# Kernel optimization log

Hardware: AMD Instinct MI355X
Metric: run time of the kernel (lower is better)

## Reference

```python
import jax, jax.numpy as jnp
import numpy as np
import math

N_EMBD = 1024
BLOCK_SIZE = 2048
B = 4

def setup_inputs() -> dict:
    key = jax.random.key(0)
    ks = jax.random.split(key, 9)
    s = 0.02
    return {
        "q": jax.random.normal(ks[0], (B, BLOCK_SIZE, N_EMBD), jnp.float32),
        "k": jax.random.normal(ks[1], (B, BLOCK_SIZE, N_EMBD), jnp.float32),
        "v": jax.random.normal(ks[2], (B, BLOCK_SIZE, N_EMBD), jnp.float32),
        "wq_w": jax.random.normal(ks[3], (N_EMBD, N_EMBD), jnp.float32) * s,
        "wq_b": jax.random.normal(ks[4], (N_EMBD,), jnp.float32) * s,
        "wk_w": jax.random.normal(ks[5], (N_EMBD, N_EMBD), jnp.float32) * s,
        "wk_b": jax.random.normal(ks[6], (N_EMBD,), jnp.float32) * s,
        "wv_w": jax.random.normal(ks[7], (N_EMBD, N_EMBD), jnp.float32) * s,
        "wv_b": jax.random.normal(ks[8], (N_EMBD,), jnp.float32) * s,
        "causal": 1,
    }

def reference(q, k, v, wq_w, wq_b, wk_w, wk_b, wv_w, wv_b, causal):
    # torch Linear: y = x @ W.T + b
    qp = jnp.einsum('bte,oe->bto', q, wq_w) + wq_b
    kp = jnp.einsum('bte,oe->bto', k, wk_w) + wk_b
    vp = jnp.einsum('bte,oe->bto', v, wv_w) + wv_b
    scale = 1.0 / math.sqrt(N_EMBD)
    weights = jnp.einsum('bqe,bke->bqk', qp, kp) * scale  # [B,T1,T2]
    if causal:
        T1, T2 = qp.shape[1], kp.shape[1]
        mask = jnp.tril(jnp.ones((T1, T2), dtype=bool))
        weights = jnp.where(mask, weights, -jnp.inf)
    attn = jax.nn.softmax(weights, axis=-1)
    return jnp.einsum('bqk,bke->bqe', attn, vp)
```

## Files before the change

### kernel.cpp

```cpp
#include <hip/hip_runtime.h>
#include <hip/hip_bf16.h>
#include <cstdint>
#include <math.h>

#define T 2048
#define NE 1024
#define NB 4

typedef __attribute__((ext_vector_type(8))) short short8;
typedef __attribute__((ext_vector_type(4))) float floatx4;

__device__ __forceinline__ unsigned short f2bf(float f) {
    unsigned u = __float_as_uint(f);
    u += 0x7FFF + ((u >> 16) & 1);
    return (unsigned short)(u >> 16);
}

__device__ __forceinline__ short8 cvt8(floatx4 f0, floatx4 f1) {
    __hip_bfloat162 a = __float22bfloat162_rn(float2{f0[0], f0[1]});
    __hip_bfloat162 b = __float22bfloat162_rn(float2{f0[2], f0[3]});
    __hip_bfloat162 c = __float22bfloat162_rn(float2{f1[0], f1[1]});
    __hip_bfloat162 d = __float22bfloat162_rn(float2{f1[2], f1[3]});
    union { short8 s; unsigned u[4]; } r;
    r.u[0] = *(unsigned*)&a; r.u[1] = *(unsigned*)&b;
    r.u[2] = *(unsigned*)&c; r.u[3] = *(unsigned*)&d;
    return r.s;
}

__device__ __forceinline__ void gl2lds(const void* g, void* l) {
    __builtin_amdgcn_global_load_lds(
        (const __attribute__((address_space(1))) void*)g,
        (__attribute__((address_space(3))) void*)l, 16, 0, 0);
}

template<int BIAS_MODE, bool OUT_F32, bool CKLIM, bool DUAL, int MODE>
__global__ __launch_bounds__(256) void gemm_bf16(
    const unsigned short* __restrict__ A0, const unsigned short* __restrict__ A1,
    const unsigned short* __restrict__ B0, const unsigned short* __restrict__ B1,
    const float* __restrict__ bias0, const float* __restrict__ bias1,
    void* __restrict__ C0, void* __restrict__ C1,
    int K, int lda, int ldb, int ldc,
    size_t sA, size_t sB, size_t sC, float scale)
{
    int tm, tn;
    const int bz = blockIdx.z;
    if (MODE == 2) {
        const int i = blockIdx.x;
        int lin = (i & 7) * 17 + (i >> 3);
        tm = (int)((sqrtf(8.f * (float)lin + 1.f) - 1.f) * 0.5f);
        while ((tm + 1) * (tm + 2) / 2 <= lin) ++tm;
        while (tm * (tm + 1) / 2 > lin) --tm;
        tn = lin - tm * (tm + 1) / 2;
    } else if (MODE == 1) {
        const int bid = blockIdx.x;
        const int lin = (bid & 7) * (gridDim.x >> 3) + (bid >> 3);
        tm = lin >> 3; tn = lin & 7;
    } else if (MODE == 3) {
        const int xcd = blockIdx.x & 7, j = blockIdx.x >> 3;
        tm = (j & 1) ? xcd : (15 - xcd);
        tn = j >> 1;
    } else {
        tn = blockIdx.x; tm = blockIdx.y;
    }

    __shared__ __align__(16) char As[16384];
    __shared__ __align__(16) char Bs[16384];

    const int tid = threadIdx.x, lane = tid & 63, wave = tid >> 6;
    const int wm = wave & 1, wn = wave >> 1;
    const int quad = lane >> 4, l15 = lane & 15;

    const char* Ab = (const char*)((DUAL && bz) ? A1 : A0) + (size_t)bz * sA * 2;
    const char* Bb = (const char*)((DUAL && bz) ? B1 : B0) + (size_t)bz * sB * 2;
    const float* bias = (DUAL && bz) ? bias1 : bias0;

    int Keff = K;
    if (CKLIM) { int kl = (tm + 1) * 128; Keff = kl < K ? kl : K; }

    const size_t ldab = (size_t)lda * 2, ldbb = (size_t)ldb * 2;
    const char* gA = Ab + (size_t)(tm * 128 + wave * 8 + (lane >> 3)) * ldab + (size_t)(lane & 7) * 16;
    const char* gB = Bb + (size_t)(tn * 128 + wave * 8 + (lane >> 3)) * ldbb + (size_t)(lane & 7) * 16;
    char* lA = As + wave * 1024;
    char* lB = Bs + wave * 1024;

    floatx4 acc[4][4] = {};

    for (int k0 = 0; k0 < Keff; k0 += 64) {
        const size_t kb = (size_t)k0 * 2;
        #pragma unroll
        for (int c = 0; c < 4; ++c)
            gl2lds(gA + (size_t)c * 32 * ldab + kb, lA + c * 4096);
        #pragma unroll
        for (int c = 0; c < 4; ++c)
            gl2lds(gB + (size_t)c * 32 * ldbb + kb, lB + c * 4096);
        __syncthreads();

        #pragma unroll
        for (int kk = 0; kk < 2; kk++) {
            short8 af[4], bfr[4];
            #pragma unroll
            for (int i = 0; i < 4; i++)
                af[i] = *(const short8*)(As + (wm * 64 + i * 16 + l15) * 128 + kk * 64 + quad * 16);
            #pragma unroll
            for (int j = 0; j < 4; j++)
                bfr[j] = *(const short8*)(Bs + (wn * 64 + j * 16 + l15) * 128 + kk * 64 + quad * 16);
            #pragma unroll
            for (int i = 0; i < 4; i++)
                #pragma unroll
                for (int j = 0; j < 4; j++)
                    acc[i][j] = __builtin_amdgcn_mfma_f32_16x16x32_bf16(af[i], bfr[j], acc[i][j], 0, 0, 0);
        }
        __syncthreads();
    }

    char* Cb = (char*)((DUAL && bz) ? C1 : C0) + (size_t)bz * sC * (OUT_F32 ? 4 : 2);
    #pragma unroll
    for (int i = 0; i < 4; i++) {
        #pragma unroll
        for (int j = 0; j < 4; j++) {
            const int n = tn * 128 + wn * 64 + j * 16 + l15;
            #pragma unroll
            for (int r = 0; r < 4; r++) {
                const int m = tm * 128 + wm * 64 + i * 16 + quad * 4 + r;
                float val = acc[i][j][r] * scale;
                if (BIAS_MODE == 1) val += bias[n];
                if (BIAS_MODE == 2) val += bias[m];
                if (OUT_F32) ((float*)Cb)[(size_t)m * ldc + n] = val;
                else         ((unsigned short*)Cb)[(size_t)m * ldc + n] = f2bf(val);
            }
        }
    }
}

__global__ __launch_bounds__(256) void cvt_all(
    const float* __restrict__ q, const float* __restrict__ k, const float* __restrict__ v,
    const float* __restrict__ wq, const float* __restrict__ wk, const float* __restrict__ wv,
    unsigned short* __restrict__ qb, unsigned short* __restrict__ kb, unsigned short* __restrict__ vb,
    unsigned short* __restrict__ wqb, unsigned short* __restrict__ wkb, unsigned short* __restrict__ wvb)
{
    const int IN8 = NB * T * NE / 8;
    const int W8  = NE * NE / 8;
    int i = blockIdx.x * 256 + threadIdx.x;
    const float* s; unsigned short* d; int j;
    if (i < 3 * IN8) {
        int sel = i / IN8; j = i - sel * IN8;
        s = sel == 0 ? q : sel == 1 ? k : v;
        d = sel == 0 ? qb : sel == 1 ? kb : vb;
    } else {
        int t2 = i - 3 * IN8; int sel = t2 / W8; j = t2 - sel * W8;
        s = sel == 0 ? wq : sel == 1 ? wk : wv;
        d = sel == 0 ? wqb : sel == 1 ? wkb : wvb;
    }
    const floatx4* p = (const floatx4*)s;
    ((short8*)d)[j] = cvt8(p[2 * j], p[2 * j + 1]);
}

__global__ __launch_bounds__(256) void softmax_causal(unsigned short* __restrict__ S)
{
    const int row = blockIdx.x;
    const int b = row >> 11, r = row & 2047;
    unsigned short* p = S + ((size_t)b * T + (size_t)r) * T;
    const int nv = r + 1;
    const int lim = ((r >> 7) + 1) * 128;
    const int tid = threadIdx.x, lane = tid & 63, wave = tid >> 6;
    const int c0 = tid * 8;
    const bool act = c0 < lim;

    short8 raw = {};
    if (act) raw = ((const short8*)p)[tid];
    float x[8];
    float mx = -3.0e38f;
    #pragma unroll
    for (int j = 0; j < 8; j++) {
        float vv = -3.0e38f;
        if (c0 + j < nv) vv = __uint_as_float((unsigned)(unsigned short)raw[j] << 16);
        x[j] = vv;
        mx = fmaxf(mx, vv);
    }
    #pragma unroll
    for (int off = 32; off > 0; off >>= 1)
        mx = fmaxf(mx, __shfl_xor(mx, off));
    __shared__ float smax[4], ssum[4];
    if (lane == 0) smax[wave] = mx;
    __syncthreads();
    mx = fmaxf(fmaxf(smax[0], smax[1]), fmaxf(smax[2], smax[3]));

    float s = 0.f;
    #pragma unroll
    for (int j = 0; j < 8; j++) {
        float e = 0.f;
        if (c0 + j < nv) e = __expf(x[j] - mx);
        x[j] = e;
        s += e;
    }
    #pragma unroll
    for (int off = 32; off > 0; off >>= 1)
        s += __shfl_xor(s, off);
    if (lane == 0) ssum[wave] = s;
    __syncthreads();
    const float inv = 1.f / (ssum[0] + ssum[1] + ssum[2] + ssum[3]);

    if (act) {
        short8 o;
        #pragma unroll
        for (int j = 0; j < 8; j++)
            o[j] = (short)f2bf(x[j] * inv);
        ((short8*)p)[tid] = o;
    }
}

extern "C" void kernel_launch(void* const* d_in, const int* in_sizes, int n_in,
                              void* d_out, int out_size, void* d_ws, size_t ws_size,
                              hipStream_t stream)
{
    const float* q    = (const float*)d_in[0];
    const float* k    = (const float*)d_in[1];
    const float* v    = (const float*)d_in[2];
    const float* wq_w = (const float*)d_in[3];
    const float* wq_b = (const float*)d_in[4];
    const float* wk_w = (const float*)d_in[5];
    const float* wk_b = (const float*)d_in[6];
    const float* wv_w = (const float*)d_in[7];
    const float* wv_b = (const float*)d_in[8];

    const size_t INEL = (size_t)NB * T * NE;

    unsigned short* qp = (unsigned short*)d_out;
    unsigned short* kp = qp + INEL;

    unsigned short* vpT = (unsigned short*)d_ws;
    unsigned short* S   = vpT + (size_t)NB * NE * T;
    unsigned short* qb  = S;
    unsigned short* kb  = qb + INEL;
    unsigned short* vb  = kb + INEL;
    unsigned short* wqb = vb + INEL;
    unsigned short* wkb = wqb + (size_t)NE * NE;
    unsigned short* wvb = wkb + (size_t)NE * NE;

    dim3 blk(256);

    const int NCVT = (3 * (int)(INEL / 8) + 3 * NE * NE / 8 + 255) / 256;
    cvt_all<<<dim3(NCVT), blk, 0, stream>>>(q, k, v, wq_w, wk_w, wv_w, qb, kb, vb, wqb, wkb, wvb);

    gemm_bf16<1, false, false, true, 1><<<dim3(512, 1, 2), blk, 0, stream>>>(
        qb, kb, wqb, wkb, wq_b, wk_b, qp, kp, NE, NE, NE, NE, 0, 0, 0, 1.0f);

    gemm_bf16<2, false, false, false, 0><<<dim3(T/128, NE/128, NB), blk, 0, stream>>>(
        wvb, nullptr, vb, nullptr, wv_b, nullptr, vpT, nullptr,
        NE, NE, NE, T, 0, (size_t)T * NE, (size_t)NE * T, 1.0f);

    gemm_bf16<0, false, false, false, 2><<<dim3(136, 1, NB), blk, 0, stream>>>(
        qp, nullptr, kp, nullptr, nullptr, nullptr, S, nullptr,
        NE, NE, NE, T, (size_t)T * NE, (size_t)T * NE, (size_t)T * T, 0.03125f);

    softmax_causal<<<dim3(NB * T), blk, 0, stream>>>(S);

    gemm_bf16<0, true, true, false, 3><<<dim3(128, 1, NB), blk, 0, stream>>>(
        S, nullptr, vpT, nullptr, nullptr, nullptr, d_out, nullptr,
        T, T, T, NE, (size_t)T * T, (size_t)NE * T, (size_t)T * NE, 1.0f);
}
```

Baseline: 343.7 us.

## Swizzle LDS tiles with XOR and use 256x128 tiles for projection GEMMs

LDS chunk positions are XOR-swizzled by row so the MFMA fragment reads avoid bank conflicts. The GEMM is parameterised by waves per row, and the Q/K and V projection GEMMs now use 512-thread blocks with 256-row A tiles. This raises B-tile reuse and cuts the block count. The risk is fewer blocks for the V projection and higher register or LDS pressure per block.

```diff
diff --git a/kernel.cpp b/kernel.cpp
--- a/kernel.cpp
+++ b/kernel.cpp
@@ -33,15 +33,16 @@
         (__attribute__((address_space(3))) void*)l, 16, 0, 0);
 }
 
-template<int BIAS_MODE, bool OUT_F32, bool CKLIM, bool DUAL, int MODE>
-__global__ __launch_bounds__(256) void gemm_bf16(
+template<int NWROW, int BIAS_MODE, bool OUT_F32, bool CKLIM, bool DUAL, int MODE>
+__global__ __launch_bounds__(NWROW * 128, 4) void gemm_bf16(
     const unsigned short* __restrict__ A0, const unsigned short* __restrict__ A1,
     const unsigned short* __restrict__ B0, const unsigned short* __restrict__ B1,
     const float* __restrict__ bias0, const float* __restrict__ bias1,
     void* __restrict__ C0, void* __restrict__ C1,
     int K, int lda, int ldb, int ldc,
-    size_t sA, size_t sB, size_t sC, float scale)
-{
+    size_t sA, size_t sB, size_t sC, float scale, int ntnShift)
+{
+    constexpr int NTHR = NWROW * 128;
     int tm, tn;
     const int bz = blockIdx.z;
     if (MODE == 2) {
@@ -54,7 +55,7 @@
     } else if (MODE == 1) {
         const int bid = blockIdx.x;
         const int lin = (bid & 7) * (gridDim.x >> 3) + (bid >> 3);
-        tm = lin >> 3; tn = lin & 7;
+        tm = lin >> ntnShift; tn = lin & ((1 << ntnShift) - 1);
     } else if (MODE == 3) {
         const int xcd = blockIdx.x & 7, j = blockIdx.x >> 3;
         tm = (j & 1) ? xcd : (15 - xcd);
@@ -63,12 +64,14 @@
         tn = blockIdx.x; tm = blockIdx.y;
     }
 
-    __shared__ __align__(16) char As[16384];
-    __shared__ __align__(16) char Bs[16384];
+    __shared__ __align__(16) char As[NWROW * 64 * 128];
+    __shared__ __align__(16) char Bs[128 * 128];
 
     const int tid = threadIdx.x, lane = tid & 63, wave = tid >> 6;
-    const int wm = wave & 1, wn = wave >> 1;
+    const int wm = wave % NWROW, wn = wave / NWROW;
     const int quad = lane >> 4, l15 = lane & 15;
+    const int p = l15 & 7;
+    const int r8 = lane >> 3, c8 = lane & 7;
 
     const char* Ab = (const char*)((DUAL && bz) ? A1 : A0) + (size_t)bz * sA * 2;
     const char* Bb = (const char*)((DUAL && bz) ? B1 : B0) + (size_t)bz * sB * 2;
@@ -78,10 +81,11 @@
     if (CKLIM) { int kl = (tm + 1) * 128; Keff = kl < K ? kl : K; }
 
     const size_t ldab = (size_t)lda * 2, ldbb = (size_t)ldb * 2;
-    const char* gA = Ab + (size_t)(tm * 128 + wave * 8 + (lane >> 3)) * ldab + (size_t)(lane & 7) * 16;
-    const char* gB = Bb + (size_t)(tn * 128 + wave * 8 + (lane >> 3)) * ldbb + (size_t)(lane & 7) * 16;
+    const char* gA = Ab + (size_t)(tm * (NWROW * 64) + wave * 8 + r8) * ldab + (size_t)((c8 ^ r8) * 16);
+    const char* gB = Bb + (size_t)(tn * 128 + wave * 8 + r8) * ldbb + (size_t)((c8 ^ r8) * 16);
     char* lA = As + wave * 1024;
     char* lB = Bs + wave * 1024;
+    constexpr int BCALLS = 8 / NWROW;
 
     floatx4 acc[4][4] = {};
 
@@ -89,10 +93,10 @@
         const size_t kb = (size_t)k0 * 2;
         #pragma unroll
         for (int c = 0; c < 4; ++c)
-            gl2lds(gA + (size_t)c * 32 * ldab + kb, lA + c * 4096);
-        #pragma unroll
-        for (int c = 0; c < 4; ++c)
-            gl2lds(gB + (size_t)c * 32 * ldbb + kb, lB + c * 4096);
+            gl2lds(gA + (size_t)(c * NWROW * 16) * ldab + kb, lA + c * NTHR * 16);
+        #pragma unroll
+        for (int c = 0; c < BCALLS; ++c)
+            gl2lds(gB + (size_t)(c * NWROW * 16) * ldbb + kb, lB + c * NTHR * 16);
         __syncthreads();
 
         #pragma unroll
@@ -100,10 +104,10 @@
             short8 af[4], bfr[4];
             #pragma unroll
             for (int i = 0; i < 4; i++)
-                af[i] = *(const short8*)(As + (wm * 64 + i * 16 + l15) * 128 + kk * 64 + quad * 16);
+                af[i] = *(const short8*)(As + (wm * 64 + i * 16 + l15) * 128 + (((kk * 4 + quad) ^ p) << 4));
             #pragma unroll
             for (int j = 0; j < 4; j++)
-                bfr[j] = *(const short8*)(Bs + (wn * 64 + j * 16 + l15) * 128 + kk * 64 + quad * 16);
+                bfr[j] = *(const short8*)(Bs + (wn * 64 + j * 16 + l15) * 128 + (((kk * 4 + quad) ^ p) << 4));
             #pragma unroll
             for (int i = 0; i < 4; i++)
                 #pragma unroll
@@ -121,7 +125,7 @@
             const int n = tn * 128 + wn * 64 + j * 16 + l15;
             #pragma unroll
             for (int r = 0; r < 4; r++) {
-                const int m = tm * 128 + wm * 64 + i * 16 + quad * 4 + r;
+                const int m = tm * (NWROW * 64) + wm * 64 + i * 16 + quad * 4 + r;
                 float val = acc[i][j][r] * scale;
                 if (BIAS_MODE == 1) val += bias[n];
                 if (BIAS_MODE == 2) val += bias[m];
@@ -151,8 +155,8 @@
         s = sel == 0 ? wq : sel == 1 ? wk : wv;
         d = sel == 0 ? wqb : sel == 1 ? wkb : wvb;
     }
-    const floatx4* p = (const floatx4*)s;
-    ((short8*)d)[j] = cvt8(p[2 * j], p[2 * j + 1]);
+    const floatx4* pp = (const floatx4*)s;
+    ((short8*)d)[j] = cvt8(pp[2 * j], pp[2 * j + 1]);
 }
 
 __global__ __launch_bounds__(256) void softmax_causal(unsigned short* __restrict__ S)
@@ -242,20 +246,20 @@
     const int NCVT = (3 * (int)(INEL / 8) + 3 * NE * NE / 8 + 255) / 256;
     cvt_all<<<dim3(NCVT), blk, 0, stream>>>(q, k, v, wq_w, wk_w, wv_w, qb, kb, vb, wqb, wkb, wvb);
 
-    gemm_bf16<1, false, false, true, 1><<<dim3(512, 1, 2), blk, 0, stream>>>(
-        qb, kb, wqb, wkb, wq_b, wk_b, qp, kp, NE, NE, NE, NE, 0, 0, 0, 1.0f);
-
-    gemm_bf16<2, false, false, false, 0><<<dim3(T/128, NE/128, NB), blk, 0, stream>>>(
+    gemm_bf16<4, 1, false, false, true, 1><<<dim3(256, 1, 2), dim3(512), 0, stream>>>(
+        qb, kb, wqb, wkb, wq_b, wk_b, qp, kp, NE, NE, NE, NE, 0, 0, 0, 1.0f, 3);
+
+    gemm_bf16<4, 2, false, false, false, 1><<<dim3(64, 1, NB), dim3(512), 0, stream>>>(
         wvb, nullptr, vb, nullptr, wv_b, nullptr, vpT, nullptr,
-        NE, NE, NE, T, 0, (size_t)T * NE, (size_t)NE * T, 1.0f);
-
-    gemm_bf16<0, false, false, false, 2><<<dim3(136, 1, NB), blk, 0, stream>>>(
+        NE, NE, NE, T, 0, (size_t)T * NE, (size_t)NE * T, 1.0f, 4);
+
+    gemm_bf16<2, 0, false, false, false, 2><<<dim3(136, 1, NB), blk, 0, stream>>>(
         qp, nullptr, kp, nullptr, nullptr, nullptr, S, nullptr,
-        NE, NE, NE, T, (size_t)T * NE, (size_t)T * NE, (size_t)T * T, 0.03125f);
+        NE, NE, NE, T, (size_t)T * NE, (size_t)T * NE, (size_t)T * T, 0.03125f, 0);
 
     softmax_causal<<<dim3(NB * T), blk, 0, stream>>>(S);
 
-    gemm_bf16<0, true, true, false, 3><<<dim3(128, 1, NB), blk, 0, stream>>>(
+    gemm_bf16<2, 0, true, true, false, 3><<<dim3(128, 1, NB), blk, 0, stream>>>(
         S, nullptr, vpT, nullptr, nullptr, nullptr, d_out, nullptr,
-        T, T, T, NE, (size_t)T * T, (size_t)NE * T, (size_t)T * NE, 1.0f);
-}
+        T, T, T, NE, (size_t)T * T, (size_t)NE * T, (size_t)T * NE, 1.0f, 0);
+}
```

Result: faster. 298.3 us (-13.2%).
